# Performance work log

Measured on AMD Instinct MI355X. Metric: run time of the kernel, lower is better.

The kernel has to match this reference:

```python
import jax, jax.numpy as jnp
from jax import lax
import numpy as np

VQ_DIM = 64
VQ_NUM = 512


def conv1d(x, w, b=None, stride=1, pad=0):
    # x: (N, C, L), w: (O, I, K) torch Conv1d layout
    y = lax.conv_general_dilated(x, w, (stride,), [(pad, pad)],
                                 dimension_numbers=('NCH', 'OIH', 'NCH'))
    return y if b is None else y + b[None, :, None]


def convT1d(x, w, b=None, stride=1, pad=0):
    # w: (I, O, K) torch ConvTranspose1d layout; emulate via input-dilated conv
    k = w.shape[2]
    w2 = jnp.flip(w, 2).transpose(1, 0, 2)  # -> (O, I, K)
    y = lax.conv_general_dilated(x, w2, (1,), [(k - 1 - pad, k - 1 - pad)],
                                 lhs_dilation=(stride,),
                                 dimension_numbers=('NCH', 'OIH', 'NCH'))
    return y if b is None else y + b[None, :, None]


def bn(x, g, b, eps=1e-5):
    # training-mode BatchNorm1d: batch stats over (N, L), biased variance
    mu = x.mean((0, 2), keepdims=True)
    var = x.var((0, 2), keepdims=True)
    return g[None, :, None] * (x - mu) * lax.rsqrt(var + eps) + b[None, :, None]


def setup_inputs() -> dict:
    key = jax.random.key(0)
    ks = iter(jax.random.split(key, 64))

    def rn(shape, s=0.05):
        return jax.random.normal(next(ks), shape, jnp.float32) * s

    inp = {}
    inp['x'] = jax.random.normal(next(ks), (64, 32, 1024), jnp.float32)
    inp['w_conv'] = rn((64, 32, 7)); inp['b_conv'] = rn((64,))
    inp['g_conv'] = jnp.ones((64,), jnp.float32); inp['be_conv'] = jnp.zeros((64,), jnp.float32)
    inp['w_r1'] = rn((3, 64, 64, 3)); inp['b_r1'] = rn((3, 64))
    inp['g_r1'] = jnp.ones((3, 64), jnp.float32); inp['be_r1'] = jnp.zeros((3, 64), jnp.float32)
    inp['w_ds1'] = rn((64, 64, 2)); inp['b_ds1'] = rn((64,))
    inp['w_r2'] = rn((128, 64, 3)); inp['b_r2'] = rn((128,))
    inp['g_r2'] = jnp.ones((128,), jnp.float32); inp['be_r2'] = jnp.zeros((128,), jnp.float32)
    inp['w_1to2'] = rn((128, 64, 1))
    inp['w_ds2'] = rn((128, 128, 2)); inp['b_ds2'] = rn((128,))
    initrange = 1.0 / VQ_NUM
    inp['embed_w'] = jax.random.uniform(next(ks), (VQ_NUM, VQ_DIM), jnp.float32,
                                        minval=-initrange, maxval=initrange)
    inp['w_us2'] = rn((128, 128, 2)); inp['b_us2'] = rn((128,))
    inp['w_dr2'] = rn((128, 64, 3)); inp['b_dr2'] = rn((64,))
    inp['g_dr2'] = jnp.ones((64,), jnp.float32); inp['be_dr2'] = jnp.zeros((64,), jnp.float32)
    inp['w_2to1'] = rn((64, 128, 1))
    inp['w_us1'] = rn((64, 64, 2)); inp['b_us1'] = rn((64,))
    inp['w_dr1'] = rn((3, 64, 64, 3)); inp['b_dr1'] = rn((3, 64))
    inp['g_dr1'] = jnp.ones((3, 64), jnp.float32); inp['be_dr1'] = jnp.zeros((3, 64), jnp.float32)
    inp['w_deconv'] = rn((64, 32, 7)); inp['b_deconv'] = rn((32,))
    return inp


def reference(x, w_conv, b_conv, g_conv, be_conv, w_r1, b_r1, g_r1, be_r1,
              w_ds1, b_ds1, w_r2, b_r2, g_r2, be_r2, w_1to2, w_ds2, b_ds2,
              embed_w, w_us2, b_us2, w_dr2, b_dr2, g_dr2, be_dr2, w_2to1,
              w_us1, b_us1, w_dr1, b_dr1, g_dr1, be_dr1, w_deconv, b_deconv):
    # ---- encoder ----
    h = bn(conv1d(x, w_conv, b_conv, pad=3), g_conv, be_conv)
    r = h
    for i in range(3):
        r = bn(conv1d(r, w_r1[i], b_r1[i], pad=1), g_r1[i], be_r1[i])
        if i < 2:
            r = jax.nn.relu(r)
    h = h + r                                  # res1 skip
    h = conv1d(h, w_ds1, b_ds1, stride=2)      # L -> L/2
    r = bn(conv1d(h, w_r2, b_r2, pad=1), g_r2, be_r2)
    h = conv1d(h, w_1to2) + r                  # res2 skip w/ 1x1 channel map
    h = conv1d(h, w_ds2, b_ds2, stride=2)      # L/2 -> L/4
    # ---- vector quantization ----
    B, C, L = h.shape
    Z = h.reshape(-1, VQ_DIM)                  # (N, vq_dim)
    # ||z - w||^2 expanded: avoids (N, K, D) broadcast intermediate
    d = (Z * Z).sum(1, keepdims=True) - 2.0 * (Z @ embed_w.T) + (embed_w * embed_w).sum(1)[None, :]
    j = jnp.argmin(d, axis=1)
    Wj = embed_w[j]
    sg = lax.stop_gradient
    commit_loss = ((Z - sg(Wj)) ** 2).sum(1).mean()
    vq_loss = ((sg(Z) - Wj) ** 2).sum(1).mean()
    hq = Wj.reshape(B, C, L)
    # ---- decoder ----
    t = convT1d(hq, w_us2, b_us2, stride=2)    # L/4 -> L/2
    r = bn(convT1d(t, w_dr2, b_dr2, pad=1), g_dr2, be_dr2)
    t = conv1d(t, w_2to1) + r
    t = convT1d(t, w_us1, b_us1, stride=2)     # L/2 -> L
    r = t
    for i in range(3):
        r = bn(convT1d(r, w_dr1[i], b_dr1[i], pad=1), g_dr1[i], be_dr1[i])
        if i < 2:
            r = jax.nn.relu(r)
    t = t + r
    out = convT1d(t, w_deconv, b_deconv, pad=3)
    return out, commit_loss, vq_loss
```

## Files before the change

### kernel.cpp

```cpp
#include <hip/hip_runtime.h>
#include <stdint.h>

#define F_WT     1
#define F_STATS  2
#define F_BIAS   4
#define F_INBN   8
#define F_INRELU 16
#define F_INB    32
#define F_INBBN  64
#define F_ADD    128
#define F_ADDBN  256

template<int CI, int CO, int K, int MODE, int TL, int COB, int FLAGS>
__global__ __launch_bounds__(256)
void conv_rE(const float* __restrict__ xa, const float2* __restrict__ sca,
             const float* __restrict__ xb, const float2* __restrict__ scb,
             const float* __restrict__ w,  const float* __restrict__ bias,
             const float* __restrict__ addsrc, const float2* __restrict__ scadd,
             double* __restrict__ stats, float* __restrict__ yout,
             int Lin, int Lout, int pad, int cis, int wci)
{
    constexpr int CR   = 2;
    constexpr int NCG  = COB / CR;
    constexpr int LT   = 256 / NCG;
    constexpr int TLT  = TL / LT;
    constexpr int SPAN = (MODE == 0) ? (TL + K - 1)
                       : (MODE == 1) ? ((TL - 1) * 2 + K)
                       : (TL / 2);
    constexpr int SPANP = (SPAN + 3) & ~3;
    constexpr int WN    = COB * CI * K;
    constexpr int XR    = (MODE == 0) ? (TLT + K - 1)
                        : (MODE == 1) ? ((TLT - 1) * 2 + K)
                        : (TLT / 2);
    constexpr int WR    = K * CR;
    constexpr bool SWZ  = (MODE == 0 && TLT == 8) || (MODE == 1 && TLT == 4);

    __shared__ float xs[CI * SPANP];
    __shared__ float wl[WN];

    const int tid    = threadIdx.x;
    const int ltile  = blockIdx.x;
    const int n      = blockIdx.y;
    const int coBase = blockIdx.z * COB;

    for (int i = tid; i < WN; i += 256) {
        int ci   = i / (K * COB);
        int rem  = i - ci * (K * COB);
        int k    = rem / COB;
        int co_l = rem - k * COB;
        int co   = coBase + co_l;
        int src;
        if (FLAGS & F_WT)   src = (ci * CO + co) * K + (K - 1 - k);
        else if (MODE == 2) src = (ci * CO + co) * K + k;
        else                src = (co * wci + ci) * K + k;
        wl[i] = w[src];
    }

    int x0;
    if (MODE == 0)      x0 = ltile * TL - pad;
    else if (MODE == 1) x0 = ltile * TL * 2;
    else                x0 = ltile * (TL / 2);

    for (int i = tid; i < CI * SPAN; i += 256) {
        int ci = i / SPAN;
        int s  = i - ci * SPAN;
        int xl = x0 + s;
        float v = 0.f;
        if (xl >= 0 && xl < Lin) {
            size_t idx = ((size_t)n * cis + ci) * (size_t)Lin + xl;
            v = xa[idx];
            if (FLAGS & F_INBN)   { float2 t = sca[ci]; v = v * t.x + t.y; }
            if (FLAGS & F_INRELU) v = fmaxf(v, 0.f);
            if (FLAGS & F_INB) {
                float u = xb[idx];
                if (FLAGS & F_INBBN) { float2 t = scb[ci]; u = u * t.x + t.y; }
                v += u;
            }
        }
        int st = ci * SPANP + s;
        if (SWZ) st ^= (st >> 3) & 4;
        xs[st] = v;
    }
    __syncthreads();

    const int cog   = tid / LT;
    const int lg    = tid % LT;
    const int co0   = coBase + cog * CR;
    const int loOff = lg * TLT;
    const int xoff  = (MODE == 1) ? loOff * 2
                    : (MODE == 2) ? (loOff >> 1) : loOff;

    float acc[CR][TLT];
#pragma unroll
    for (int cr = 0; cr < CR; ++cr) {
        float b = (FLAGS & F_BIAS) ? bias[co0 + cr] : 0.f;
#pragma unroll
        for (int j = 0; j < TLT; ++j) acc[cr][j] = b;
    }

    float xA[XR], xB[XR], wA[WR], wB[WR];

    auto ldx = [&](float* dst, int c) {
        const int base = c * SPANP + xoff;
#pragma unroll
        for (int g = 0; g < XR; g += 4) {
            int pb = base + g;
            if (SWZ) pb ^= (pb >> 3) & 4;
            const float* p = &xs[pb];
            constexpr int GMAX = 4;
#pragma unroll
            for (int t = 0; t < GMAX; ++t)
                if (g + t < XR) dst[g + t] = p[t];
        }
    };
    auto ldw = [&](float* dst, int c) {
        const float* q = &wl[c * (K * COB) + cog * CR];
#pragma unroll
        for (int k = 0; k < K; ++k)
#pragma unroll
            for (int cr = 0; cr < CR; ++cr)
                dst[k * CR + cr] = q[k * COB + cr];
    };
    auto dofma = [&](const float* xv, const float* wv) {
        if (MODE == 2) {
#pragma unroll
            for (int j = 0; j < TLT; ++j)
#pragma unroll
                for (int cr = 0; cr < CR; ++cr)
                    acc[cr][j] += wv[(j & 1) * CR + cr] * xv[j >> 1];
        } else {
#pragma unroll
            for (int k = 0; k < K; ++k)
#pragma unroll
                for (int j = 0; j < TLT; ++j)
#pragma unroll
                    for (int cr = 0; cr < CR; ++cr)
                        acc[cr][j] += wv[k * CR + cr]
                                    * xv[((MODE == 1) ? 2 * j : j) + k];
        }
    };

    ldx(xA, 0); ldw(wA, 0);
    for (int ci = 0; ci + 2 < CI; ci += 2) {
        ldx(xB, ci + 1); ldw(wB, ci + 1);
        dofma(xA, wA);
        ldx(xA, ci + 2); ldw(wA, ci + 2);
        dofma(xB, wB);
    }
    ldx(xB, CI - 1); ldw(wB, CI - 1);
    dofma(xA, wA);
    dofma(xB, wB);

    const int lo0 = ltile * TL + loOff;
#pragma unroll
    for (int cr = 0; cr < CR; ++cr) {
        size_t ob = ((size_t)n * CO + (co0 + cr)) * (size_t)Lout + lo0;
        if (FLAGS & F_ADD) {
            float2 t = (FLAGS & F_ADDBN) ? scadd[co0 + cr] : make_float2(1.f, 0.f);
#pragma unroll
            for (int j = 0; j < TLT; ++j) {
                float a = addsrc[ob + j];
                acc[cr][j] += (FLAGS & F_ADDBN) ? (a * t.x + t.y) : a;
            }
        }
#pragma unroll
        for (int j = 0; j < TLT; ++j) yout[ob + j] = acc[cr][j];
    }

    if (FLAGS & F_STATS) {
        float s1[CR], s2[CR];
#pragma unroll
        for (int cr = 0; cr < CR; ++cr) {
            s1[cr] = 0.f; s2[cr] = 0.f;
#pragma unroll
            for (int j = 0; j < TLT; ++j) {
                s1[cr] += acc[cr][j];
                s2[cr] += acc[cr][j] * acc[cr][j];
            }
        }
#pragma unroll
        for (int m = 1; m < LT; m <<= 1) {
#pragma unroll
            for (int cr = 0; cr < CR; ++cr) {
                s1[cr] += __shfl_xor(s1[cr], m, 64);
                s2[cr] += __shfl_xor(s2[cr], m, 64);
            }
        }
        if ((tid & (LT - 1)) == 0) {
#pragma unroll
            for (int cr = 0; cr < CR; ++cr) {
                atomicAdd(&stats[co0 + cr],      (double)s1[cr]);
                atomicAdd(&stats[CO + co0 + cr], (double)s2[cr]);
            }
        }
    }
}

__global__ void bnp_rD(const double* __restrict__ stats,
                       const float* __restrict__ g, const float* __restrict__ be,
                       float2* __restrict__ sc, int C, double invNL)
{
    int c = threadIdx.x;
    if (c >= C) return;
    double mu  = stats[c] * invNL;
    double var = stats[C + c] * invNL - mu * mu;
    double rs  = 1.0 / sqrt(var + 1e-5);
    double gv  = (double)g[c] * rs;
    double bv  = (double)be[c] - mu * gv;
    sc[c] = make_float2((float)gv, (float)bv);
}

__global__ __launch_bounds__(256)
void vq_rD(const float* __restrict__ z, const float* __restrict__ emb,
           float* __restrict__ hq, double* __restrict__ lossAcc)
{
    __shared__ float ws[128 * 68];
    const int tid = threadIdx.x;
    const int sub = tid & 3;
    const int r   = blockIdx.x * 64 + (tid >> 2);

    const float4* zp = (const float4*)(z + (size_t)r * 64 + sub * 16);
    float4 z0 = zp[0], z1 = zp[1], z2 = zp[2], z3 = zp[3];

    float best = 3.4e38f;
    int   bj   = 0;
    for (int c0 = 0; c0 < 512; c0 += 128) {
        __syncthreads();
        for (int i = tid; i < 128 * 16; i += 256) {
            int j = i >> 4, q = i & 15;
            ((float4*)ws)[j * 17 + q] = ((const float4*)(emb + c0 * 64))[i];
        }
        __syncthreads();
        for (int j = 0; j < 128; ++j) {
            const float4* wp = (const float4*)&ws[j * 68 + sub * 16];
            float4 w0 = wp[0], w1 = wp[1], w2 = wp[2], w3 = wp[3];
            float d = 0.f, t;
            t = z0.x - w0.x; d += t * t;  t = z0.y - w0.y; d += t * t;
            t = z0.z - w0.z; d += t * t;  t = z0.w - w0.w; d += t * t;
            t = z1.x - w1.x; d += t * t;  t = z1.y - w1.y; d += t * t;
            t = z1.z - w1.z; d += t * t;  t = z1.w - w1.w; d += t * t;
            t = z2.x - w2.x; d += t * t;  t = z2.y - w2.y; d += t * t;
            t = z2.z - w2.z; d += t * t;  t = z2.w - w2.w; d += t * t;
            t = z3.x - w3.x; d += t * t;  t = z3.y - w3.y; d += t * t;
            t = z3.z - w3.z; d += t * t;  t = z3.w - w3.w; d += t * t;
            d += __shfl_xor(d, 1, 64);
            d += __shfl_xor(d, 2, 64);
            if (d < best) { best = d; bj = c0 + j; }
        }
    }

    const float4* ep = (const float4*)(emb + (size_t)bj * 64 + sub * 16);
    float4* hp = (float4*)(hq + (size_t)r * 64 + sub * 16);
    hp[0] = ep[0]; hp[1] = ep[1]; hp[2] = ep[2]; hp[3] = ep[3];

    float s = (sub == 0) ? best : 0.f;
#pragma unroll
    for (int m = 1; m < 64; m <<= 1) s += __shfl_xor(s, m, 64);
    if ((tid & 63) == 0) atomicAdd(lossAcc, (double)s);
}

__global__ void zd_rD(double* p, int n) {
    int i = blockIdx.x * 256 + threadIdx.x;
    if (i < n) p[i] = 0.0;
}

__global__ void wsguard_rD(float* p, int n) {
    int i = blockIdx.x * 256 + threadIdx.x;
    if (i < n) p[i] = 1000.0f;
}

__global__ void lossfin_rD(const double* acc, float* out) {
    float m = (float)(acc[0] * (1.0 / 32768.0));
    out[2097152] = m;
    out[2097153] = m;
}

extern "C" void kernel_launch(void* const* d_in, const int* in_sizes, int n_in,
                              void* d_out, int out_size, void* d_ws, size_t ws_size,
                              hipStream_t stream)
{
    const size_t NEED = (size_t)3 * 4194304 * 4 + 2305 * 8 + 1152 * 8 + 64;
    if (ws_size < NEED) {
        wsguard_rD<<<dim3((out_size + 255) / 256), 256, 0, stream>>>((float*)d_out, out_size);
        return;
    }

    const float* x        = (const float*)d_in[0];
    const float* w_conv   = (const float*)d_in[1];
    const float* b_conv   = (const float*)d_in[2];
    const float* g_conv   = (const float*)d_in[3];
    const float* be_conv  = (const float*)d_in[4];
    const float* w_r1     = (const float*)d_in[5];
    const float* b_r1     = (const float*)d_in[6];
    const float* g_r1     = (const float*)d_in[7];
    const float* be_r1    = (const float*)d_in[8];
    const float* w_ds1    = (const float*)d_in[9];
    const float* b_ds1    = (const float*)d_in[10];
    const float* w_r2     = (const float*)d_in[11];
    const float* b_r2     = (const float*)d_in[12];
    const float* g_r2     = (const float*)d_in[13];
    const float* be_r2    = (const float*)d_in[14];
    const float* w_1to2   = (const float*)d_in[15];
    const float* w_ds2    = (const float*)d_in[16];
    const float* b_ds2    = (const float*)d_in[17];
    const float* embed_w  = (const float*)d_in[18];
    const float* w_us2    = (const float*)d_in[19];
    const float* b_us2    = (const float*)d_in[20];
    const float* w_dr2    = (const float*)d_in[21];
    const float* b_dr2    = (const float*)d_in[22];
    const float* g_dr2    = (const float*)d_in[23];
    const float* be_dr2   = (const float*)d_in[24];
    const float* w_2to1   = (const float*)d_in[25];
    const float* w_us1    = (const float*)d_in[26];
    const float* b_us1    = (const float*)d_in[27];
    const float* w_dr1    = (const float*)d_in[28];
    const float* b_dr1    = (const float*)d_in[29];
    const float* g_dr1    = (const float*)d_in[30];
    const float* be_dr1   = (const float*)d_in[31];
    const float* w_deconv = (const float*)d_in[32];
    const float* b_deconv = (const float*)d_in[33];

    float* out = (float*)d_out;

    float*  B0 = (float*)d_ws;
    float*  B1 = B0 + 4194304;
    float*  B2 = B1 + 4194304;
    double* SD = (double*)(B2 + 4194304);
    double* lossAcc = SD + 9 * 256;
    float2* SC = (float2*)(SD + 2305);

    const int N = 64;
    const double i64k = 1.0 / 65536.0;
    const double i32k = 1.0 / 32768.0;
    const float2* NOSC = nullptr;
    const float*  NOP  = nullptr;

    zd_rD<<<dim3(10), 256, 0, stream>>>(SD, 9 * 256 + 1);

    conv_rE<32,64,7,0,128,32, F_BIAS|F_STATS>
        <<<dim3(8, N, 2), 256, 0, stream>>>(x, NOSC, NOP, NOSC, w_conv, b_conv,
            NOP, NOSC, SD+0*256, B0, 1024, 1024, 3, 32, 32);
    bnp_rD<<<1, 128, 0, stream>>>(SD+0*256, g_conv, be_conv, SC+0*128, 64, i64k);

    conv_rE<64,64,3,0,128,32, F_BIAS|F_STATS|F_INBN>
        <<<dim3(8, N, 2), 256, 0, stream>>>(B0, SC+0*128, NOP, NOSC, w_r1, b_r1,
            NOP, NOSC, SD+1*256, B1, 1024, 1024, 1, 64, 64);
    bnp_rD<<<1, 128, 0, stream>>>(SD+1*256, g_r1, be_r1, SC+1*128, 64, i64k);

    conv_rE<64,64,3,0,128,32, F_BIAS|F_STATS|F_INBN|F_INRELU>
        <<<dim3(8, N, 2), 256, 0, stream>>>(B1, SC+1*128, NOP, NOSC, w_r1+12288, b_r1+64,
            NOP, NOSC, SD+2*256, B2, 1024, 1024, 1, 64, 64);
    bnp_rD<<<1, 128, 0, stream>>>(SD+2*256, g_r1+64, be_r1+64, SC+2*128, 64, i64k);

    conv_rE<64,64,3,0,128,32, F_BIAS|F_STATS|F_INBN|F_INRELU>
        <<<dim3(8, N, 2), 256, 0, stream>>>(B2, SC+2*128, NOP, NOSC, w_r1+24576, b_r1+128,
            NOP, NOSC, SD+3*256, B1, 1024, 1024, 1, 64, 64);
    bnp_rD<<<1, 128, 0, stream>>>(SD+3*256, g_r1+128, be_r1+128, SC+3*128, 64, i64k);

    conv_rE<64,64,2,1,64,32, F_BIAS|F_INBN|F_INB|F_INBBN>
        <<<dim3(8, N, 2), 256, 0, stream>>>(B1, SC+3*128, B0, SC+0*128, w_ds1, b_ds1,
            NOP, NOSC, nullptr, B2, 1024, 512, 0, 64, 64);

    conv_rE<64,128,3,0,128,32, F_BIAS|F_STATS>
        <<<dim3(4, N, 4), 256, 0, stream>>>(B2, NOSC, NOP, NOSC, w_r2, b_r2,
            NOP, NOSC, SD+4*256, B1, 512, 512, 1, 64, 64);
    bnp_rD<<<1, 128, 0, stream>>>(SD+4*256, g_r2, be_r2, SC+4*128, 128, i32k);

    conv_rE<64,128,1,0,128,32, F_ADD|F_ADDBN>
        <<<dim3(4, N, 4), 256, 0, stream>>>(B2, NOSC, NOP, NOSC, w_1to2, NOP,
            B1, SC+4*128, nullptr, B0, 512, 512, 0, 64, 64);

    conv_rE<128,128,2,1,32,32, F_BIAS>
        <<<dim3(8, N, 4), 256, 0, stream>>>(B0, NOSC, NOP, NOSC, w_ds2, b_ds2,
            NOP, NOSC, nullptr, B1, 512, 256, 0, 128, 128);

    vq_rD<<<dim3(512), 256, 0, stream>>>(B1, embed_w, B2, lossAcc);
    lossfin_rD<<<1, 1, 0, stream>>>(lossAcc, out);

    conv_rE<128,128,2,2,128,32, F_BIAS>
        <<<dim3(4, N, 4), 256, 0, stream>>>(B2, NOSC, NOP, NOSC, w_us2, b_us2,
            NOP, NOSC, nullptr, B0, 256, 512, 0, 128, 128);

    conv_rE<64,64,3,0,128,32, F_WT|F_BIAS>
        <<<dim3(4, N, 2), 256, 0, stream>>>(B0, NOSC, NOP, NOSC, w_dr2, b_dr2,
            NOP, NOSC, nullptr, B1, 512, 512, 1, 128, 64);
    conv_rE<64,64,3,0,128,32, F_WT|F_STATS|F_ADD>
        <<<dim3(4, N, 2), 256, 0, stream>>>(B0 + (size_t)64*512, NOSC, NOP, NOSC,
            w_dr2 + 64*64*3, NOP, B1, NOSC, SD+5*256, B1, 512, 512, 1, 128, 64);
    bnp_rD<<<1, 128, 0, stream>>>(SD+5*256, g_dr2, be_dr2, SC+5*128, 64, i32k);

    conv_rE<64,64,1,0,128,32, F_ADD|F_ADDBN>
        <<<dim3(4, N, 2), 256, 0, stream>>>(B0, NOSC, NOP, NOSC, w_2to1, NOP,
            B1, SC+5*128, nullptr, B2, 512, 512, 0, 128, 128);
    conv_rE<64,64,1,0,128,32, F_ADD>
        <<<dim3(4, N, 2), 256, 0, stream>>>(B0 + (size_t)64*512, NOSC, NOP, NOSC,
            w_2to1 + 64, NOP, B2, NOSC, nullptr, B2, 512, 512, 0, 128, 128);

    conv_rE<64,64,2,2,128,32, F_BIAS>
        <<<dim3(8, N, 2), 256, 0, stream>>>(B2, NOSC, NOP, NOSC, w_us1, b_us1,
            NOP, NOSC, nullptr, B0, 512, 1024, 0, 64, 64);

    conv_rE<64,64,3,0,128,32, F_WT|F_BIAS|F_STATS>
        <<<dim3(8, N, 2), 256, 0, stream>>>(B0, NOSC, NOP, NOSC, w_dr1, b_dr1,
            NOP, NOSC, SD+6*256, B1, 1024, 1024, 1, 64, 64);
    bnp_rD<<<1, 128, 0, stream>>>(SD+6*256, g_dr1, be_dr1, SC+6*128, 64, i64k);

    conv_rE<64,64,3,0,128,32, F_WT|F_BIAS|F_STATS|F_INBN|F_INRELU>
        <<<dim3(8, N, 2), 256, 0, stream>>>(B1, SC+6*128, NOP, NOSC, w_dr1+12288, b_dr1+64,
            NOP, NOSC, SD+7*256, B2, 1024, 1024, 1, 64, 64);
    bnp_rD<<<1, 128, 0, stream>>>(SD+7*256, g_dr1+64, be_dr1+64, SC+7*128, 64, i64k);

    conv_rE<64,64,3,0,128,32, F_WT|F_BIAS|F_STATS|F_INBN|F_INRELU>
        <<<dim3(8, N, 2), 256, 0, stream>>>(B2, SC+7*128, NOP, NOSC, w_dr1+24576, b_dr1+128,
            NOP, NOSC, SD+8*256, B1, 1024, 1024, 1, 64, 64);
    bnp_rD<<<1, 128, 0, stream>>>(SD+8*256, g_dr1+128, be_dr1+128, SC+8*128, 64, i64k);

    conv_rE<64,32,7,0,64,32, F_WT|F_BIAS|F_INBN|F_INB>
        <<<dim3(16, N, 1), 256, 0, stream>>>(B1, SC+8*128, B0, NOSC, w_deconv, b_deconv,
            NOP, NOSC, nullptr, out, 1024, 1024, 3, 64, 64);
}
```

Baseline: 1.220 ms.

## Retile conv kernels with per-thread weight rows and split VQ argmin

The conv kernel takes the output-channel register block CR as a template parameter and now lays weights out in shared memory as contiguous per-channel-group rows. Most stride-1 convs switch to 256-wide length tiles with 16 channels per block and 4 channels per thread, which raises register reuse of the x loads. Epilogue adds and stores are vectorised to float4. The VQ step uses a dot-product distance with precomputed codebook norms and is split across two half-codebook kernels plus a merge kernel, which adds parallelism but also an extra launch, scratch buffers and more register pressure.

Result: slower. 1.655 ms (+35.6%).

```diff
diff --git a/kernel.cpp b/kernel.cpp
--- a/kernel.cpp
+++ b/kernel.cpp
@@ -11,16 +11,15 @@
 #define F_ADD    128
 #define F_ADDBN  256
 
-template<int CI, int CO, int K, int MODE, int TL, int COB, int FLAGS>
+template<int CI, int CO, int K, int MODE, int TL, int COB, int CR, int FLAGS>
 __global__ __launch_bounds__(256)
-void conv_rE(const float* __restrict__ xa, const float2* __restrict__ sca,
+void conv_rF(const float* __restrict__ xa, const float2* __restrict__ sca,
              const float* __restrict__ xb, const float2* __restrict__ scb,
              const float* __restrict__ w,  const float* __restrict__ bias,
              const float* __restrict__ addsrc, const float2* __restrict__ scadd,
              double* __restrict__ stats, float* __restrict__ yout,
              int Lin, int Lout, int pad, int cis, int wci)
 {
-    constexpr int CR   = 2;
     constexpr int NCG  = COB / CR;
     constexpr int LT   = 256 / NCG;
     constexpr int TLT  = TL / LT;
@@ -28,32 +27,35 @@
                        : (MODE == 1) ? ((TL - 1) * 2 + K)
                        : (TL / 2);
     constexpr int SPANP = (SPAN + 3) & ~3;
-    constexpr int WN    = COB * CI * K;
+    constexpr int WR    = K * CR;
+    constexpr int WRP   = (WR + 3) & ~3;
+    constexpr int WROW  = CI * WRP + 4;
     constexpr int XR    = (MODE == 0) ? (TLT + K - 1)
                         : (MODE == 1) ? ((TLT - 1) * 2 + K)
                         : (TLT / 2);
-    constexpr int WR    = K * CR;
     constexpr bool SWZ  = (MODE == 0 && TLT == 8) || (MODE == 1 && TLT == 4);
 
     __shared__ float xs[CI * SPANP];
-    __shared__ float wl[WN];
+    __shared__ float wl[NCG * WROW];
 
     const int tid    = threadIdx.x;
     const int ltile  = blockIdx.x;
     const int n      = blockIdx.y;
     const int coBase = blockIdx.z * COB;
 
-    for (int i = tid; i < WN; i += 256) {
-        int ci   = i / (K * COB);
-        int rem  = i - ci * (K * COB);
-        int k    = rem / COB;
-        int co_l = rem - k * COB;
-        int co   = coBase + co_l;
+    for (int i = tid; i < NCG * CI * WR; i += 256) {
+        int cogi = i / (CI * WR);
+        int rem  = i - cogi * (CI * WR);
+        int ci   = rem / WR;
+        int rem2 = rem - ci * WR;
+        int k    = rem2 / CR;
+        int cr   = rem2 - k * CR;
+        int co   = coBase + cogi * CR + cr;
         int src;
         if (FLAGS & F_WT)   src = (ci * CO + co) * K + (K - 1 - k);
         else if (MODE == 2) src = (ci * CO + co) * K + k;
         else                src = (co * wci + ci) * K + k;
-        wl[i] = w[src];
+        wl[cogi * WROW + ci * WRP + k * CR + cr] = w[src];
     }
 
     int x0;
@@ -107,19 +109,15 @@
             int pb = base + g;
             if (SWZ) pb ^= (pb >> 3) & 4;
             const float* p = &xs[pb];
-            constexpr int GMAX = 4;
-#pragma unroll
-            for (int t = 0; t < GMAX; ++t)
+#pragma unroll
+            for (int t = 0; t < 4; ++t)
                 if (g + t < XR) dst[g + t] = p[t];
         }
     };
     auto ldw = [&](float* dst, int c) {
-        const float* q = &wl[c * (K * COB) + cog * CR];
-#pragma unroll
-        for (int k = 0; k < K; ++k)
-#pragma unroll
-            for (int cr = 0; cr < CR; ++cr)
-                dst[k * CR + cr] = q[k * COB + cr];
+        const float* q = &wl[cog * WROW + c * WRP];
+#pragma unroll
+        for (int t = 0; t < WR; ++t) dst[t] = q[t];
     };
     auto dofma = [&](const float* xv, const float* wv) {
         if (MODE == 2) {
@@ -157,14 +155,37 @@
         size_t ob = ((size_t)n * CO + (co0 + cr)) * (size_t)Lout + lo0;
         if (FLAGS & F_ADD) {
             float2 t = (FLAGS & F_ADDBN) ? scadd[co0 + cr] : make_float2(1.f, 0.f);
-#pragma unroll
-            for (int j = 0; j < TLT; ++j) {
-                float a = addsrc[ob + j];
-                acc[cr][j] += (FLAGS & F_ADDBN) ? (a * t.x + t.y) : a;
+            if constexpr (TLT % 4 == 0) {
+#pragma unroll
+                for (int jv = 0; jv < TLT / 4; ++jv) {
+                    float4 av = ((const float4*)(addsrc + ob))[jv];
+                    float* a4 = &acc[cr][jv * 4];
+                    if (FLAGS & F_ADDBN) {
+                        a4[0] += av.x * t.x + t.y; a4[1] += av.y * t.x + t.y;
+                        a4[2] += av.z * t.x + t.y; a4[3] += av.w * t.x + t.y;
+                    } else {
+                        a4[0] += av.x; a4[1] += av.y; a4[2] += av.z; a4[3] += av.w;
+                    }
+                }
+            } else {
+#pragma unroll
+                for (int j = 0; j < TLT; ++j) {
+                    float a = addsrc[ob + j];
+                    acc[cr][j] += (FLAGS & F_ADDBN) ? (a * t.x + t.y) : a;
+                }
             }
         }
-#pragma unroll
-        for (int j = 0; j < TLT; ++j) yout[ob + j] = acc[cr][j];
+        if constexpr (TLT % 4 == 0) {
+#pragma unroll
+            for (int jv = 0; jv < TLT / 4; ++jv) {
+                float4 sv = make_float4(acc[cr][jv*4+0], acc[cr][jv*4+1],
+                                        acc[cr][jv*4+2], acc[cr][jv*4+3]);
+                ((float4*)(yout + ob))[jv] = sv;
+            }
+        } else {
+#pragma unroll
+            for (int j = 0; j < TLT; ++j) yout[ob + j] = acc[cr][j];
+        }
     }
 
     if (FLAGS & F_STATS) {
@@ -211,52 +232,105 @@
 }
 
 __global__ __launch_bounds__(256)
-void vq_rD(const float* __restrict__ z, const float* __restrict__ emb,
-           float* __restrict__ hq, double* __restrict__ lossAcc)
+void vq1_rF(const float* __restrict__ z, const float* __restrict__ emb,
+            float* __restrict__ d0, float* __restrict__ d1,
+            int* __restrict__ j0, int* __restrict__ j1)
 {
     __shared__ float ws[128 * 68];
-    const int tid = threadIdx.x;
-    const int sub = tid & 3;
-    const int r   = blockIdx.x * 64 + (tid >> 2);
+    const int tid  = threadIdx.x;
+    const int sub  = tid & 3;
+    const int half = blockIdx.x & 1;
+    const int r    = (blockIdx.x >> 1) * 64 + (tid >> 2);
 
     const float4* zp = (const float4*)(z + (size_t)r * 64 + sub * 16);
     float4 z0 = zp[0], z1 = zp[1], z2 = zp[2], z3 = zp[3];
 
+    float zzp = 0.f;
+    zzp = fmaf(z0.x,z0.x,zzp); zzp = fmaf(z0.y,z0.y,zzp);
+    zzp = fmaf(z0.z,z0.z,zzp); zzp = fmaf(z0.w,z0.w,zzp);
+    zzp = fmaf(z1.x,z1.x,zzp); zzp = fmaf(z1.y,z1.y,zzp);
+    zzp = fmaf(z1.z,z1.z,zzp); zzp = fmaf(z1.w,z1.w,zzp);
+    zzp = fmaf(z2.x,z2.x,zzp); zzp = fmaf(z2.y,z2.y,zzp);
+    zzp = fmaf(z2.z,z2.z,zzp); zzp = fmaf(z2.w,z2.w,zzp);
+    zzp = fmaf(z3.x,z3.x,zzp); zzp = fmaf(z3.y,z3.y,zzp);
+    zzp = fmaf(z3.z,z3.z,zzp); zzp = fmaf(z3.w,z3.w,zzp);
+
     float best = 3.4e38f;
     int   bj   = 0;
-    for (int c0 = 0; c0 < 512; c0 += 128) {
+    for (int cc = 0; cc < 2; ++cc) {
+        const int c0 = half * 256 + cc * 128;
         __syncthreads();
         for (int i = tid; i < 128 * 16; i += 256) {
             int j = i >> 4, q = i & 15;
             ((float4*)ws)[j * 17 + q] = ((const float4*)(emb + c0 * 64))[i];
         }
         __syncthreads();
+        for (int i = tid; i < 512; i += 256) {
+            int j = i >> 2, s = i & 3;
+            const float4* p = (const float4*)&ws[j * 68 + s * 16];
+            float4 a = p[0], b = p[1], c = p[2], d = p[3];
+            float ww = 0.f;
+            ww = fmaf(a.x,a.x,ww); ww = fmaf(a.y,a.y,ww);
+            ww = fmaf(a.z,a.z,ww); ww = fmaf(a.w,a.w,ww);
+            ww = fmaf(b.x,b.x,ww); ww = fmaf(b.y,b.y,ww);
+            ww = fmaf(b.z,b.z,ww); ww = fmaf(b.w,b.w,ww);
+            ww = fmaf(c.x,c.x,ww); ww = fmaf(c.y,c.y,ww);
+            ww = fmaf(c.z,c.z,ww); ww = fmaf(c.w,c.w,ww);
+            ww = fmaf(d.x,d.x,ww); ww = fmaf(d.y,d.y,ww);
+            ww = fmaf(d.z,d.z,ww); ww = fmaf(d.w,d.w,ww);
+            ws[j * 68 + 64 + s] = ww;
+        }
+        __syncthreads();
         for (int j = 0; j < 128; ++j) {
             const float4* wp = (const float4*)&ws[j * 68 + sub * 16];
             float4 w0 = wp[0], w1 = wp[1], w2 = wp[2], w3 = wp[3];
-            float d = 0.f, t;
-            t = z0.x - w0.x; d += t * t;  t = z0.y - w0.y; d += t * t;
-            t = z0.z - w0.z; d += t * t;  t = z0.w - w0.w; d += t * t;
-            t = z1.x - w1.x; d += t * t;  t = z1.y - w1.y; d += t * t;
-            t = z1.z - w1.z; d += t * t;  t = z1.w - w1.w; d += t * t;
-            t = z2.x - w2.x; d += t * t;  t = z2.y - w2.y; d += t * t;
-            t = z2.z - w2.z; d += t * t;  t = z2.w - w2.w; d += t * t;
-            t = z3.x - w3.x; d += t * t;  t = z3.y - w3.y; d += t * t;
-            t = z3.z - w3.z; d += t * t;  t = z3.w - w3.w; d += t * t;
-            d += __shfl_xor(d, 1, 64);
-            d += __shfl_xor(d, 2, 64);
-            if (d < best) { best = d; bj = c0 + j; }
-        }
-    }
-
-    const float4* ep = (const float4*)(emb + (size_t)bj * 64 + sub * 16);
-    float4* hp = (float4*)(hq + (size_t)r * 64 + sub * 16);
-    hp[0] = ep[0]; hp[1] = ep[1]; hp[2] = ep[2]; hp[3] = ep[3];
-
-    float s = (sub == 0) ? best : 0.f;
+            float dot = 0.f;
+            dot = fmaf(z0.x,w0.x,dot); dot = fmaf(z0.y,w0.y,dot);
+            dot = fmaf(z0.z,w0.z,dot); dot = fmaf(z0.w,w0.w,dot);
+            dot = fmaf(z1.x,w1.x,dot); dot = fmaf(z1.y,w1.y,dot);
+            dot = fmaf(z1.z,w1.z,dot); dot = fmaf(z1.w,w1.w,dot);
+            dot = fmaf(z2.x,w2.x,dot); dot = fmaf(z2.y,w2.y,dot);
+            dot = fmaf(z2.z,w2.z,dot); dot = fmaf(z2.w,w2.w,dot);
+            dot = fmaf(z3.x,w3.x,dot); dot = fmaf(z3.y,w3.y,dot);
+            dot = fmaf(z3.z,w3.z,dot); dot = fmaf(z3.w,w3.w,dot);
+            float t = fmaf(dot, -2.f, ws[j * 68 + 64 + sub]);
+            t += __shfl_xor(t, 1, 64);
+            t += __shfl_xor(t, 2, 64);
+            if (t < best) { best = t; bj = c0 + j; }
+        }
+    }
+
+    float zz = zzp;
+    zz += __shfl_xor(zz, 1, 64);
+    zz += __shfl_xor(zz, 2, 64);
+
+    if (sub == 0) {
+        if (half) { d1[r] = zz + best; j1[r] = bj; }
+        else      { d0[r] = zz + best; j0[r] = bj; }
+    }
+}
+
+__global__ __launch_bounds__(256)
+void vq2_rF(const float* __restrict__ d0, const float* __restrict__ d1,
+            const int* __restrict__ j0, const int* __restrict__ j1,
+            const float* __restrict__ emb, float* __restrict__ hq,
+            double* __restrict__ lossAcc)
+{
+    const int r = blockIdx.x * 256 + threadIdx.x;
+    float da = d0[r], db = d1[r];
+    bool pick1 = db < da;
+    float d = pick1 ? db : da;
+    int   j = pick1 ? j1[r] : j0[r];
+
+    const float4* ep = (const float4*)(emb + (size_t)j * 64);
+    float4* hp = (float4*)(hq + (size_t)r * 64);
+#pragma unroll
+    for (int t = 0; t < 16; ++t) hp[t] = ep[t];
+
+    float s = d;
 #pragma unroll
     for (int m = 1; m < 64; m <<= 1) s += __shfl_xor(s, m, 64);
-    if ((tid & 63) == 0) atomicAdd(lossAcc, (double)s);
+    if ((threadIdx.x & 63) == 0) atomicAdd(lossAcc, (double)s);
 }
 
 __global__ void zd_rD(double* p, int n) {
@@ -329,6 +403,11 @@
     double* lossAcc = SD + 9 * 256;
     float2* SC = (float2*)(SD + 2305);
 
+    float* vqd0 = B0;
+    float* vqd1 = B0 + 32768;
+    int*   vqj0 = (int*)(B0 + 65536);
+    int*   vqj1 = (int*)(B0 + 98304);
+
     const int N = 64;
     const double i64k = 1.0 / 65536.0;
     const double i32k = 1.0 / 32768.0;
@@ -337,85 +416,86 @@
 
     zd_rD<<<dim3(10), 256, 0, stream>>>(SD, 9 * 256 + 1);
 
-    conv_rE<32,64,7,0,128,32, F_BIAS|F_STATS>
-        <<<dim3(8, N, 2), 256, 0, stream>>>(x, NOSC, NOP, NOSC, w_conv, b_conv,
+    conv_rF<32,64,7,0,256,16,4, F_BIAS|F_STATS>
+        <<<dim3(4, N, 4), 256, 0, stream>>>(x, NOSC, NOP, NOSC, w_conv, b_conv,
             NOP, NOSC, SD+0*256, B0, 1024, 1024, 3, 32, 32);
     bnp_rD<<<1, 128, 0, stream>>>(SD+0*256, g_conv, be_conv, SC+0*128, 64, i64k);
 
-    conv_rE<64,64,3,0,128,32, F_BIAS|F_STATS|F_INBN>
-        <<<dim3(8, N, 2), 256, 0, stream>>>(B0, SC+0*128, NOP, NOSC, w_r1, b_r1,
+    conv_rF<64,64,3,0,256,16,4, F_BIAS|F_STATS|F_INBN>
+        <<<dim3(4, N, 4), 256, 0, stream>>>(B0, SC+0*128, NOP, NOSC, w_r1, b_r1,
             NOP, NOSC, SD+1*256, B1, 1024, 1024, 1, 64, 64);
     bnp_rD<<<1, 128, 0, stream>>>(SD+1*256, g_r1, be_r1, SC+1*128, 64, i64k);
 
-    conv_rE<64,64,3,0,128,32, F_BIAS|F_STATS|F_INBN|F_INRELU>
-        <<<dim3(8, N, 2), 256, 0, stream>>>(B1, SC+1*128, NOP, NOSC, w_r1+12288, b_r1+64,
+    conv_rF<64,64,3,0,256,16,4, F_BIAS|F_STATS|F_INBN|F_INRELU>
+        <<<dim3(4, N, 4), 256, 0, stream>>>(B1, SC+1*128, NOP, NOSC, w_r1+12288, b_r1+64,
             NOP, NOSC, SD+2*256, B2, 1024, 1024, 1, 64, 64);
     bnp_rD<<<1, 128, 0, stream>>>(SD+2*256, g_r1+64, be_r1+64, SC+2*128, 64, i64k);
 
-    conv_rE<64,64,3,0,128,32, F_BIAS|F_STATS|F_INBN|F_INRELU>
-        <<<dim3(8, N, 2), 256, 0, stream>>>(B2, SC+2*128, NOP, NOSC, w_r1+24576, b_r1+128,
+    conv_rF<64,64,3,0,256,16,4, F_BIAS|F_STATS|F_INBN|F_INRELU>
+        <<<dim3(4, N, 4), 256, 0, stream>>>(B2, SC+2*128, NOP, NOSC, w_r1+24576, b_r1+128,
             NOP, NOSC, SD+3*256, B1, 1024, 1024, 1, 64, 64);
     bnp_rD<<<1, 128, 0, stream>>>(SD+3*256, g_r1+128, be_r1+128, SC+3*128, 64, i64k);
 
-    conv_rE<64,64,2,1,64,32, F_BIAS|F_INBN|F_INB|F_INBBN>
+    conv_rF<64,64,2,1,64,32,2, F_BIAS|F_INBN|F_INB|F_INBBN>
         <<<dim3(8, N, 2), 256, 0, stream>>>(B1, SC+3*128, B0, SC+0*128, w_ds1, b_ds1,
             NOP, NOSC, nullptr, B2, 1024, 512, 0, 64, 64);
 
-    conv_rE<64,128,3,0,128,32, F_BIAS|F_STATS>
-        <<<dim3(4, N, 4), 256, 0, stream>>>(B2, NOSC, NOP, NOSC, w_r2, b_r2,
+    conv_rF<64,128,3,0,256,16,4, F_BIAS|F_STATS>
+        <<<dim3(2, N, 8), 256, 0, stream>>>(B2, NOSC, NOP, NOSC, w_r2, b_r2,
             NOP, NOSC, SD+4*256, B1, 512, 512, 1, 64, 64);
     bnp_rD<<<1, 128, 0, stream>>>(SD+4*256, g_r2, be_r2, SC+4*128, 128, i32k);
 
-    conv_rE<64,128,1,0,128,32, F_ADD|F_ADDBN>
-        <<<dim3(4, N, 4), 256, 0, stream>>>(B2, NOSC, NOP, NOSC, w_1to2, NOP,
+    conv_rF<64,128,1,0,256,16,4, F_ADD|F_ADDBN>
+        <<<dim3(2, N, 8), 256, 0, stream>>>(B2, NOSC, NOP, NOSC, w_1to2, NOP,
             B1, SC+4*128, nullptr, B0, 512, 512, 0, 64, 64);
 
-    conv_rE<128,128,2,1,32,32, F_BIAS>
+    conv_rF<128,128,2,1,32,32,2, F_BIAS>
         <<<dim3(8, N, 4), 256, 0, stream>>>(B0, NOSC, NOP, NOSC, w_ds2, b_ds2,
             NOP, NOSC, nullptr, B1, 512, 256, 0, 128, 128);
 
-    vq_rD<<<dim3(512), 256, 0, stream>>>(B1, embed_w, B2, lossAcc);
+    vq1_rF<<<dim3(1024), 256, 0, stream>>>(B1, embed_w, vqd0, vqd1, vqj0, vqj1);
+    vq2_rF<<<dim3(128), 256, 0, stream>>>(vqd0, vqd1, vqj0, vqj1, embed_w, B2, lossAcc);
     lossfin_rD<<<1, 1, 0, stream>>>(lossAcc, out);
 
-    conv_rE<128,128,2,2,128,32, F_BIAS>
+    conv_rF<128,128,2,2,128,32,2, F_BIAS>
         <<<dim3(4, N, 4), 256, 0, stream>>>(B2, NOSC, NOP, NOSC, w_us2, b_us2,
             NOP, NOSC, nullptr, B0, 256, 512, 0, 128, 128);
 
-    conv_rE<64,64,3,0,128,32, F_WT|F_BIAS>
-        <<<dim3(4, N, 2), 256, 0, stream>>>(B0, NOSC, NOP, NOSC, w_dr2, b_dr2,
+    conv_rF<64,64,3,0,256,16,4, F_WT|F_BIAS>
+        <<<dim3(2, N, 4), 256, 0, stream>>>(B0, NOSC, NOP, NOSC, w_dr2, b_dr2,
             NOP, NOSC, nullptr, B1, 512, 512, 1, 128, 64);
-    conv_rE<64,64,3,0,128,32, F_WT|F_STATS|F_ADD>
-        <<<dim3(4, N, 2), 256, 0, stream>>>(B0 + (size_t)64*512, NOSC, NOP, NOSC,
+    conv_rF<64,64,3,0,256,16,4, F_WT|F_STATS|F_ADD>
+        <<<dim3(2, N, 4), 256, 0, stream>>>(B0 + (size_t)64*512, NOSC, NOP, NOSC,
             w_dr2 + 64*64*3, NOP, B1, NOSC, SD+5*256, B1, 512, 512, 1, 128, 64);
     bnp_rD<<<1, 128, 0, stream>>>(SD+5*256, g_dr2, be_dr2, SC+5*128, 64, i32k);
 
-    conv_rE<64,64,1,0,128,32, F_ADD|F_ADDBN>
-        <<<dim3(4, N, 2), 256, 0, stream>>>(B0, NOSC, NOP, NOSC, w_2to1, NOP,
+    conv_rF<64,64,1,0,256,16,4, F_ADD|F_ADDBN>
+        <<<dim3(2, N, 4), 256, 0, stream>>>(B0, NOSC, NOP, NOSC, w_2to1, NOP,
             B1, SC+5*128, nullptr, B2, 512, 512, 0, 128, 128);
-    conv_rE<64,64,1,0,128,32, F_ADD>
-        <<<dim3(4, N, 2), 256, 0, stream>>>(B0 + (size_t)64*512, NOSC, NOP, NOSC,
+    conv_rF<64,64,1,0,256,16,4, F_ADD>
+        <<<dim3(2, N, 4), 256, 0, stream>>>(B0 + (size_t)64*512, NOSC, NOP, NOSC,
             w_2to1 + 64, NOP, B2, NOSC, nullptr, B2, 512, 512, 0, 128, 128);
 
-    conv_rE<64,64,2,2,128,32, F_BIAS>
+    conv_rF<64,64,2,2,128,32,2, F_BIAS>
         <<<dim3(8, N, 2), 256, 0, stream>>>(B2, NOSC, NOP, NOSC, w_us1, b_us1,
             NOP, NOSC, nullptr, B0, 512, 1024, 0, 64, 64);
 
-    conv_rE<64,64,3,0,128,32, F_WT|F_BIAS|F_STATS>
-        <<<dim3(8, N, 2), 256, 0, stream>>>(B0, NOSC, NOP, NOSC, w_dr1, b_dr1,
+    conv_rF<64,64,3,0,256,16,4, F_WT|F_BIAS|F_STATS>
+        <<<dim3(4, N, 4), 256, 0, stream>>>(B0, NOSC, NOP, NOSC, w_dr1, b_dr1,
             NOP, NOSC, SD+6*256, B1, 1024, 1024, 1, 64, 64);
     bnp_rD<<<1, 128, 0, stream>>>(SD+6*256, g_dr1, be_dr1, SC+6*128, 64, i64k);
 
-    conv_rE<64,64,3,0,128,32, F_WT|F_BIAS|F_STATS|F_INBN|F_INRELU>
-        <<<dim3(8, N, 2), 256, 0, stream>>>(B1, SC+6*128, NOP, NOSC, w_dr1+12288, b_dr1+64,
+    conv_rF<64,64,3,0,256,16,4, F_WT|F_BIAS|F_STATS|F_INBN|F_INRELU>
+        <<<dim3(4, N, 4), 256, 0, stream>>>(B1, SC+6*128, NOP, NOSC, w_dr1+12288, b_dr1+64,
             NOP, NOSC, SD+7*256, B2, 1024, 1024, 1, 64, 64);
     bnp_rD<<<1, 128, 0, stream>>>(SD+7*256, g_dr1+64, be_dr1+64, SC+7*128, 64, i64k);
 
-    conv_rE<64,64,3,0,128,32, F_WT|F_BIAS|F_STATS|F_INBN|F_INRELU>
-        <<<dim3(8, N, 2), 256, 0, stream>>>(B2, SC+7*128, NOP, NOSC, w_dr1+24576, b_dr1+128,
+    conv_rF<64,64,3,0,256,16,4, F_WT|F_BIAS|F_STATS|F_INBN|F_INRELU>
+        <<<dim3(4, N, 4), 256, 0, stream>>>(B2, SC+7*128, NOP, NOSC, w_dr1+24576, b_dr1+128,
             NOP, NOSC, SD+8*256, B1, 1024, 1024, 1, 64, 64);
     bnp_rD<<<1, 128, 0, stream>>>(SD+8*256, g_dr1+128, be_dr1+128, SC+8*128, 64, i64k);
 
-    conv_rE<64,32,7,0,64,32, F_WT|F_BIAS|F_INBN|F_INB>
-        <<<dim3(16, N, 1), 256, 0, stream>>>(B1, SC+8*128, B0, NOSC, w_deconv, b_deconv,
+    conv_rF<64,32,7,0,256,16,4, F_WT|F_BIAS|F_INBN|F_INB>
+        <<<dim3(4, N, 2), 256, 0, stream>>>(B1, SC+8*128, B0, NOSC, w_deconv, b_deconv,
             NOP, NOSC, nullptr, out, 1024, 1024, 3, 64, 64);
 }
```
